# Optimization experiments

Measured on AMD Instinct MI355X. Metric: run time of the kernel, lower is better.

The kernel has to match this reference:

```python
import jax, jax.numpy as jnp
import numpy as np

B, N, K, E, H, V = 128, 256, 4, 300, 150, 32000  # batch, nodes/tree, max children, embed, hidden, vocab
DELTA = 1.0


def setup_inputs() -> dict:
    key = jax.random.key(0)
    ks = jax.random.split(key, 8)
    query = jax.random.randint(ks[0], (B, N), 0, V, dtype=jnp.int32)
    pos = jax.random.randint(ks[1], (B, N), 0, V, dtype=jnp.int32)
    neg = jax.random.randint(ks[2], (B, N), 0, V, dtype=jnp.int32)
    # Complete K-ary tree over N nodes: children of node t are {K*t+1, ..., K*t+K} < N; root = node 0.
    ch = np.full((N, K), -1, dtype=np.int32)
    for t in range(N):
        for j in range(K):
            c = K * t + 1 + j
            if c < N:
                ch[t, j] = c
    children = jnp.asarray(ch)
    emb = jax.random.normal(ks[3], (V, E), dtype=jnp.float32) * 0.02
    W_iou = jax.random.normal(ks[4], (E, 3 * H), dtype=jnp.float32) * 0.05
    U_iou = jax.random.normal(ks[5], (H, 3 * H), dtype=jnp.float32) * 0.05
    b_iou = jnp.zeros((3 * H,), jnp.float32)
    W_f = jax.random.normal(ks[6], (E, H), dtype=jnp.float32) * 0.05
    U_f = jax.random.normal(ks[7], (H, H), dtype=jnp.float32) * 0.05
    b_f = jnp.zeros((H,), jnp.float32)
    return {"query": query, "pos": pos, "neg": neg, "children": children,
            "emb": emb, "W_iou": W_iou, "U_iou": U_iou, "b_iou": b_iou,
            "W_f": W_f, "U_f": U_f, "b_f": b_f}


def _childsum_treelstm(x, children, W_iou, U_iou, b_iou, W_f, U_f, b_f):
    """x: [B, N, E] node embeddings. Returns root (c, h): each [B, H]."""
    Bn, Nn, _ = x.shape
    Hh = U_f.shape[0]
    h0 = jnp.zeros((Bn, Nn, Hh), x.dtype)
    c0 = jnp.zeros((Bn, Nn, Hh), x.dtype)

    def step(carry, t):
        h_all, c_all = carry
        ch = children[t]                        # [K] child indices, -1 = padding
        mask = (ch >= 0)
        idx = jnp.where(mask, ch, 0)
        m = mask.astype(x.dtype)[None, :, None]  # [1, K, 1]
        h_k = h_all[:, idx] * m                 # [B, K, H]
        c_k = c_all[:, idx] * m
        h_sum = h_k.sum(axis=1)                 # child-sum h_tilde [B, H]
        x_t = x[:, t]                           # [B, E]
        iou = x_t @ W_iou + h_sum @ U_iou + b_iou
        i, o, u = jnp.split(iou, 3, axis=-1)
        i = jax.nn.sigmoid(i)
        o = jax.nn.sigmoid(o)
        u = jnp.tanh(u)
        # per-child forget gates: f_jk = sigmoid(W_f x_j + U_f h_k + b_f)
        f = jax.nn.sigmoid((x_t @ W_f + b_f)[:, None, :] + h_k @ U_f)  # [B, K, H]
        c_t = i * u + (f * c_k).sum(axis=1)     # c_k already masked
        h_t = o * jnp.tanh(c_t)
        return (h_all.at[:, t].set(h_t), c_all.at[:, t].set(c_t)), None

    # children have larger indices than parents -> process N-1 .. 0 (root last)
    (h_all, c_all), _ = jax.lax.scan(step, (h0, c0), jnp.arange(Nn - 1, -1, -1))
    return c_all[:, 0], h_all[:, 0]


def _cosine(a, b):
    num = (a * b).sum(-1)
    den = jnp.sqrt((a * a).sum(-1) * (b * b).sum(-1)) + 1e-8
    return num / den


def reference(query, pos, neg, children, emb, W_iou, U_iou, b_iou, W_f, U_f, b_f):
    qc, _ = _childsum_treelstm(emb[query], children, W_iou, U_iou, b_iou, W_f, U_f, b_f)
    pc, _ = _childsum_treelstm(emb[pos], children, W_iou, U_iou, b_iou, W_f, U_f, b_f)
    nc, _ = _childsum_treelstm(emb[neg], children, W_iou, U_iou, b_iou, W_f, U_f, b_f)
    a = _cosine(qc, pc)  # [B]
    b = _cosine(qc, nc)  # [B]
    return jax.nn.relu(DELTA - a + b)
```

## Files before the change

### kernel.cpp

```cpp
#include <hip/hip_runtime.h>
#include <hip/hip_bf16.h>

typedef short short8 __attribute__((ext_vector_type(8)));
typedef float floatx4 __attribute__((ext_vector_type(4)));
typedef unsigned short ushort;

#define Bb 128
#define Nn 256
#define Hh 150
#define HK 160
#define Vv 32000
#define NROW 384
#define PROJC 600
#define NINT 64
#define ZROW (Vv + NROW * NINT)

#define WTN 640

__device__ __forceinline__ float sigf(float x) { return 1.0f / (1.0f + __expf(-x)); }
__device__ __forceinline__ float tanhf_(float x) { return 1.0f - 2.0f / (__expf(2.0f * x) + 1.0f); }
__device__ __forceinline__ float bf2f(ushort s) { union { float f; unsigned u; } v; v.u = ((unsigned)s) << 16; return v.f; }
__device__ __forceinline__ ushort f2bf(float f) { __hip_bfloat16 h = __float2bfloat16(f); return *(ushort*)&h; }

__global__ __launch_bounds__(256) void k_prep(
    const float* __restrict__ W_iou, const float* __restrict__ W_f,
    const float* __restrict__ U_iou, const float* __restrict__ U_f,
    const float* __restrict__ b_iou, const float* __restrict__ b_f,
    short* __restrict__ Wt, short* __restrict__ Uti, short* __restrict__ Utf,
    float* __restrict__ biasw, ushort* __restrict__ h_u, float* __restrict__ c_u)
{
    int idx = blockIdx.x * 256 + threadIdx.x;
    const int nWt = WTN * 320, nUi = 464 * 160, nUf = 160 * 160;
    if (idx < nWt) {
        int n = idx / 320, k = idx % 320;
        float v = 0.f;
        if (k < 300) { if (n < 450) v = W_iou[k * 450 + n]; else if (n < 600) v = W_f[k * 150 + (n - 450)]; }
        Wt[idx] = (short)f2bf(v);
    } else if (idx < nWt + nUi) {
        int i2 = idx - nWt; int n = i2 / 160, k = i2 % 160;
        float v = (k < 150 && n < 450) ? U_iou[k * 450 + n] : 0.f;
        Uti[i2] = (short)f2bf(v);
    } else if (idx < nWt + nUi + nUf) {
        int i2 = idx - nWt - nUi; int n = i2 / 160, k = i2 % 160;
        float v = (k < 150) ? U_f[k * 150 + n] : 0.f;
        Utf[i2] = (short)f2bf(v);
    } else if (idx < nWt + nUi + nUf + WTN) {
        int n = idx - nWt - nUi - nUf;
        biasw[n] = n < 450 ? b_iou[n] : (n < 600 ? b_f[n - 450] : 0.f);
    } else if (idx < nWt + nUi + nUf + WTN + HK) {
        int k = idx - (nWt + nUi + nUf + WTN);
        h_u[(long)ZROW * HK + k] = 0;
        c_u[(long)ZROW * HK + k] = 0.f;
    }
}

__global__ __launch_bounds__(256) void k_vproj(
    const float* __restrict__ emb, const short* __restrict__ Wt,
    const float* __restrict__ biasw, ushort* __restrict__ proj)
{
    __shared__ __align__(16) short As[2][32][328];
    const int tid = threadIdx.x;

    const int bid = blockIdx.x;
    const int xcd = bid & 7, li = bid >> 3;
    const int wgid = (xcd < 4 ? xcd * 63 : 252 + (xcd - 4) * 62) + li;

    const int cg = wgid % 5;
    const int rg = wgid / 5;
    const int rowbase = rg * 320;

    const int w = tid >> 6, lane = tid & 63;
    const int m = lane & 15, kq = (lane >> 4) * 8;
    const int t0 = cg * 8 + w * 2;
    const int col0 = t0 * 16 + m;
    const int col1 = col0 + 16;

    short8 bq0[10], bq1[10];
    #pragma unroll
    for (int ks = 0; ks < 10; ks++) {
        bq0[ks] = *(const short8*)(Wt + (long)col0 * 320 + kq + ks * 32);
        bq1[ks] = *(const short8*)(Wt + (long)col1 * 320 + kq + ks * 32);
    }
    const float bias0 = biasw[col0];
    const float bias1 = biasw[col1];

    for (int i = tid; i < 2 * 32 * 5; i += 256) {
        int bz = i / 160, r2 = (i % 160) / 5, kk = (i % 5) * 4;
        *(short4*)&As[bz][r2][300 + kk] = make_short4(0, 0, 0, 0);
    }

    {
        const float4* src = (const float4*)emb + (long)rowbase * 75;
        for (int i = tid; i < 2400; i += 256) {
            int r = i / 75, k0 = (i % 75) * 4;
            float4 x = src[i];
            short4 sv;
            sv.x = (short)f2bf(x.x); sv.y = (short)f2bf(x.y);
            sv.z = (short)f2bf(x.z); sv.w = (short)f2bf(x.w);
            *(short4*)&As[0][r][k0] = sv;
        }
    }
    __syncthreads();

    for (int c = 0; c < 10; c++) {
        const int buf = c & 1;

        float4 x[10];
        if (c < 9) {
            const float4* src = (const float4*)emb + (long)(rowbase + (c + 1) * 32) * 75;
            #pragma unroll
            for (int j = 0; j < 10; j++) {
                int i = tid + j * 256;
                if (i < 2400) x[j] = src[i];
            }
        }

        floatx4 a00 = {0.f,0.f,0.f,0.f}, a01 = a00, a10 = a00, a11 = a00;
        #pragma unroll
        for (int ks = 0; ks < 10; ks++) {
            short8 a0 = *(const short8*)&As[buf][m][kq + ks * 32];
            short8 a1 = *(const short8*)&As[buf][16 + m][kq + ks * 32];
            a00 = __builtin_amdgcn_mfma_f32_16x16x32_bf16(a0, bq0[ks], a00, 0, 0, 0);
            a01 = __builtin_amdgcn_mfma_f32_16x16x32_bf16(a0, bq1[ks], a01, 0, 0, 0);
            a10 = __builtin_amdgcn_mfma_f32_16x16x32_bf16(a1, bq0[ks], a10, 0, 0, 0);
            a11 = __builtin_amdgcn_mfma_f32_16x16x32_bf16(a1, bq1[ks], a11, 0, 0, 0);
        }

        {
            int v0 = rowbase + c * 32;
            int rb = (lane >> 4) * 4;
            if (col0 < PROJC) {
                #pragma unroll
                for (int reg = 0; reg < 4; reg++) {
                    proj[(long)(v0 + rb + reg) * PROJC + col0]      = f2bf(a00[reg] + bias0);
                    proj[(long)(v0 + 16 + rb + reg) * PROJC + col0] = f2bf(a10[reg] + bias0);
                }
            }
            if (col1 < PROJC) {
                #pragma unroll
                for (int reg = 0; reg < 4; reg++) {
                    proj[(long)(v0 + rb + reg) * PROJC + col1]      = f2bf(a01[reg] + bias1);
                    proj[(long)(v0 + 16 + rb + reg) * PROJC + col1] = f2bf(a11[reg] + bias1);
                }
            }
        }

        if (c < 9) {
            #pragma unroll
            for (int j = 0; j < 10; j++) {
                int i = tid + j * 256;
                if (i < 2400) {
                    int r = i / 75, k0 = (i % 75) * 4;
                    short4 sv;
                    sv.x = (short)f2bf(x[j].x); sv.y = (short)f2bf(x[j].y);
                    sv.z = (short)f2bf(x[j].z); sv.w = (short)f2bf(x[j].w);
                    *(short4*)&As[buf ^ 1][r][k0] = sv;
                }
            }
        }
        __syncthreads();
    }
}

__global__ __launch_bounds__(256) void k_vleaf(
    const ushort* __restrict__ proj, ushort* __restrict__ h_u, float* __restrict__ c_u)
{
    int idx = blockIdx.x * 256 + threadIdx.x;
    int v = idx / 20, k0 = (idx % 20) * 8;
    const ushort* pr = proj + (long)v * PROJC;
    ushort hv[8]; float cvv[8];
    #pragma unroll
    for (int e = 0; e < 8; e++) {
        int k = k0 + e;
        if (k < Hh) {
            float iv = sigf(bf2f(pr[k]));
            float ov = sigf(bf2f(pr[150 + k]));
            float uv = tanhf_(bf2f(pr[300 + k]));
            float cc = iv * uv;
            cvv[e] = cc;
            hv[e] = f2bf(ov * tanhf_(cc));
        } else { cvv[e] = 0.f; hv[e] = 0; }
    }
    *(int4*)(h_u + (long)v * HK + k0) = *(int4*)hv;
    *(float4*)(c_u + (long)v * HK + k0)     = make_float4(cvv[0], cvv[1], cvv[2], cvv[3]);
    *(float4*)(c_u + (long)v * HK + k0 + 4) = make_float4(cvv[4], cvv[5], cvv[6], cvv[7]);
}

__global__ __launch_bounds__(256) void k_level(
    int t_base, int t_cnt,
    const int* __restrict__ tq, const int* __restrict__ tp, const int* __restrict__ tn,
    const int* __restrict__ children, const ushort* __restrict__ proj,
    const short* __restrict__ Uti, const short* __restrict__ Utf,
    ushort* __restrict__ h_u, float* __restrict__ c_u)
{
    __shared__ __align__(16) short As[2][5][16][168];
    __shared__ int idx_s[2][16][4];
    __shared__ int tok_s[2][16];

    const int tid = threadIdx.x;
    const int chunk = blockIdx.x / 24;
    const int r0 = (blockIdx.x % 24) * 16;
    const int tA = t_base + chunk * 2;
    const int nT = min(2, t_base + t_cnt - tA);

    if (tid < 64 * nT) {
        int tt = tid >> 6, q = tid & 63;
        int r = q >> 2, j = q & 3;
        int t = tA + tt;
        int rg = r0 + r, g = rg >> 7, b = rg & 127;
        const int* tok = (g == 0) ? tq : (g == 1 ? tp : tn);
        int ch = children[t * 4 + j];
        int idx;
        if (ch < 0)        idx = ZROW;
        else if (ch >= 64) idx = tok[b * Nn + ch];
        else               idx = Vv + rg * NINT + ch;
        idx_s[tt][r][j] = idx;
        if (j == 0) tok_s[tt][r] = tok[b * Nn + t];
    }
    __syncthreads();

    for (int i = tid; i < 320 * nT; i += 256) {
        int tt = i / 320, i2 = i % 320;
        int r = i2 / 20, k0 = (i2 % 20) * 8;
        int4 v0 = *(const int4*)(h_u + (long)idx_s[tt][r][0] * HK + k0);
        int4 v1 = *(const int4*)(h_u + (long)idx_s[tt][r][1] * HK + k0);
        int4 v2 = *(const int4*)(h_u + (long)idx_s[tt][r][2] * HK + k0);
        int4 v3 = *(const int4*)(h_u + (long)idx_s[tt][r][3] * HK + k0);
        *(int4*)&As[tt][1][r][k0] = v0;
        *(int4*)&As[tt][2][r][k0] = v1;
        *(int4*)&As[tt][3][r][k0] = v2;
        *(int4*)&As[tt][4][r][k0] = v3;
        ushort s[8];
        const ushort* p0 = (const ushort*)&v0; const ushort* p1 = (const ushort*)&v1;
        const ushort* p2 = (const ushort*)&v2; const ushort* p3 = (const ushort*)&v3;
        #pragma unroll
        for (int e = 0; e < 8; e++)
            s[e] = f2bf(bf2f(p0[e]) + bf2f(p1[e]) + bf2f(p2[e]) + bf2f(p3[e]));
        *(int4*)&As[tt][0][r][k0] = *(int4*)s;
    }
    __syncthreads();

    const int w = tid >> 6, lane = tid & 63;
    const int m = lane & 15, kq = (lane >> 4) * 8;
    const int rbase = (lane >> 4) * 4;

    for (int nt = w; nt < 10; nt += 4) {
        int col = nt * 16 + m;

        short8 Bi[5], Bo[5], Bu[5], Bf[5];
        #pragma unroll
        for (int ks = 0; ks < 5; ks++) {
            Bi[ks] = *(const short8*)(Uti + (long)(col)       * HK + kq + ks * 32);
            Bo[ks] = *(const short8*)(Uti + (long)(150 + col) * HK + kq + ks * 32);
            Bu[ks] = *(const short8*)(Uti + (long)(300 + col) * HK + kq + ks * 32);
            Bf[ks] = *(const short8*)(Utf + (long)(col)       * HK + kq + ks * 32);
        }

        for (int tt = 0; tt < nT; ++tt) {
            int t = tA + tt;

            float pv0[4], pv1[4], pv2[4], pv3[4];
            float cu0[4], cu1[4], cu2[4], cu3[4];
            if (col < Hh) {
                #pragma unroll
                for (int reg = 0; reg < 4; reg++) {
                    const ushort* pr = proj + (long)tok_s[tt][rbase + reg] * PROJC;
                    pv0[reg] = bf2f(pr[col]);
                    pv1[reg] = bf2f(pr[150 + col]);
                    pv2[reg] = bf2f(pr[300 + col]);
                    pv3[reg] = bf2f(pr[450 + col]);
                    cu0[reg] = c_u[(long)idx_s[tt][rbase + reg][0] * HK + col];
                    cu1[reg] = c_u[(long)idx_s[tt][rbase + reg][1] * HK + col];
                    cu2[reg] = c_u[(long)idx_s[tt][rbase + reg][2] * HK + col];
                    cu3[reg] = c_u[(long)idx_s[tt][rbase + reg][3] * HK + col];
                }
            }

            floatx4 ai = {0.f,0.f,0.f,0.f}, ao = ai, au = ai;
            floatx4 af0 = ai, af1 = ai, af2 = ai, af3 = ai;
            #pragma unroll
            for (int ks = 0; ks < 5; ks++) {
                short8 asum = *(const short8*)&As[tt][0][m][kq + ks * 32];
                short8 ac0  = *(const short8*)&As[tt][1][m][kq + ks * 32];
                short8 ac1  = *(const short8*)&As[tt][2][m][kq + ks * 32];
                short8 ac2  = *(const short8*)&As[tt][3][m][kq + ks * 32];
                short8 ac3  = *(const short8*)&As[tt][4][m][kq + ks * 32];
                ai  = __builtin_amdgcn_mfma_f32_16x16x32_bf16(asum, Bi[ks], ai, 0, 0, 0);
                ao  = __builtin_amdgcn_mfma_f32_16x16x32_bf16(asum, Bo[ks], ao, 0, 0, 0);
                au  = __builtin_amdgcn_mfma_f32_16x16x32_bf16(asum, Bu[ks], au, 0, 0, 0);
                af0 = __builtin_amdgcn_mfma_f32_16x16x32_bf16(ac0,  Bf[ks], af0, 0, 0, 0);
                af1 = __builtin_amdgcn_mfma_f32_16x16x32_bf16(ac1,  Bf[ks], af1, 0, 0, 0);
                af2 = __builtin_amdgcn_mfma_f32_16x16x32_bf16(ac2,  Bf[ks], af2, 0, 0, 0);
                af3 = __builtin_amdgcn_mfma_f32_16x16x32_bf16(ac3,  Bf[ks], af3, 0, 0, 0);
            }

            if (col < Hh) {
                #pragma unroll
                for (int reg = 0; reg < 4; reg++) {
                    int rg = r0 + rbase + reg;
                    float iv = sigf(pv0[reg] + ai[reg]);
                    float ov = sigf(pv1[reg] + ao[reg]);
                    float uv = tanhf_(pv2[reg] + au[reg]);
                    float fpre = pv3[reg];
                    float cv = iv * uv;
                    cv = fmaf(sigf(fpre + af0[reg]), cu0[reg], cv);
                    cv = fmaf(sigf(fpre + af1[reg]), cu1[reg], cv);
                    cv = fmaf(sigf(fpre + af2[reg]), cu2[reg], cv);
                    cv = fmaf(sigf(fpre + af3[reg]), cu3[reg], cv);
                    long o = (long)(Vv + rg * NINT + t) * HK + col;
                    c_u[o] = cv;
                    h_u[o] = f2bf(ov * tanhf_(cv));
                }
            } else {
                #pragma unroll
                for (int reg = 0; reg < 4; reg++) {
                    long o = (long)(Vv + (r0 + rbase + reg) * NINT + t) * HK + col;
                    c_u[o] = 0.f; h_u[o] = 0;
                }
            }
        }
    }
}

__global__ __launch_bounds__(64) void k_cos(const float* __restrict__ c_u, float* __restrict__ out)
{
    int b = blockIdx.x, tid = threadIdx.x;
    const float* qc = c_u + (long)(Vv + (0 * Bb + b) * NINT) * HK;
    const float* pc = c_u + (long)(Vv + (1 * Bb + b) * NINT) * HK;
    const float* nc = c_u + (long)(Vv + (2 * Bb + b) * NINT) * HK;
    float qp = 0, qn = 0, qq = 0, pp = 0, nn2 = 0;
    for (int k = tid; k < Hh; k += 64) {
        float qv = qc[k], pv = pc[k], nv = nc[k];
        qp += qv * pv; qn += qv * nv; qq += qv * qv; pp += pv * pv; nn2 += nv * nv;
    }
    #pragma unroll
    for (int off = 32; off > 0; off >>= 1) {
        qp += __shfl_down(qp, off, 64);
        qn += __shfl_down(qn, off, 64);
        qq += __shfl_down(qq, off, 64);
        pp += __shfl_down(pp, off, 64);
        nn2 += __shfl_down(nn2, off, 64);
    }
    if (tid == 0) {
        float a = qp / (sqrtf(qq * pp) + 1e-8f);
        float d = qn / (sqrtf(qq * nn2) + 1e-8f);
        out[b] = fmaxf(0.0f, 1.0f - a + d);
    }
}

extern "C" void kernel_launch(void* const* d_in, const int* in_sizes, int n_in,
                              void* d_out, int out_size, void* d_ws, size_t ws_size,
                              hipStream_t stream)
{
    const int*   tq       = (const int*)d_in[0];
    const int*   tp       = (const int*)d_in[1];
    const int*   tn       = (const int*)d_in[2];
    const int*   children = (const int*)d_in[3];
    const float* emb      = (const float*)d_in[4];
    const float* W_iou    = (const float*)d_in[5];
    const float* U_iou    = (const float*)d_in[6];
    const float* b_iou    = (const float*)d_in[7];
    const float* W_f      = (const float*)d_in[8];
    const float* U_f      = (const float*)d_in[9];
    const float* b_f      = (const float*)d_in[10];
    float* out = (float*)d_out;

    char* ws = (char*)d_ws;
    ushort* proj  = (ushort*)ws;
    ushort* h_u   = (ushort*)(ws + 38400000);
    float*  c_u   = (float*)(ws + 56504640);
    short*  Wt    = (short*)(ws + 92713920);
    short*  Uti   = (short*)(ws + 93123520);
    short*  Utf   = (short*)(ws + 93272000);
    float*  biasw = (float*)(ws + 93323200);

    k_prep<<<1194, 256, 0, stream>>>(W_iou, W_f, U_iou, U_f, b_iou, b_f,
                                     Wt, Uti, Utf, biasw, h_u, c_u);
    k_vproj<<<500, 256, 0, stream>>>(emb, Wt, biasw, proj);
    k_vleaf<<<2500, 256, 0, stream>>>(proj, h_u, c_u);
    k_level<<<22 * 24, 256, 0, stream>>>(21, 43, tq, tp, tn, children, proj, Uti, Utf, h_u, c_u);
    k_level<<<8 * 24, 256, 0, stream>>>(5, 16, tq, tp, tn, children, proj, Uti, Utf, h_u, c_u);
    k_level<<<2 * 24, 256, 0, stream>>>(1, 4,  tq, tp, tn, children, proj, Uti, Utf, h_u, c_u);
    k_level<<<1 * 24, 256, 0, stream>>>(0, 1,  tq, tp, tn, children, proj, Uti, Utf, h_u, c_u);
    k_cos<<<Bb, 64, 0, stream>>>(c_u, out);
}
```

Before: 250.2 us.

## Rebalance level-kernel wave work, double vproj grid, coalesce prep reads

The level kernel now splits the flattened (column-tile, node) work units evenly across the four waves. U-weight fragments are reloaded only when a wave's column tile changes, and child/token indices are stored as 16-bit values in shared memory. The vocabulary projection kernel launches twice as many workgroups with half the rows each, using a simpler XCD mapping, to fill more CUs. The weight-prep kernel now reads the source weights along contiguous rows and scatters the transposed writes instead. The intent is to cut wave load imbalance and raise occupancy, at the cost of more redundant B-fragment loads per vproj block and scattered writes in prep.

Result: slower. 255.3 us (+2.1%).

```diff
diff --git a/kernel.cpp b/kernel.cpp
--- a/kernel.cpp
+++ b/kernel.cpp
@@ -30,20 +30,20 @@
     float* __restrict__ biasw, ushort* __restrict__ h_u, float* __restrict__ c_u)
 {
     int idx = blockIdx.x * 256 + threadIdx.x;
-    const int nWt = WTN * 320, nUi = 464 * 160, nUf = 160 * 160;
+    const int nWt = 320 * WTN, nUi = 160 * 464, nUf = 160 * 160;
     if (idx < nWt) {
-        int n = idx / 320, k = idx % 320;
+        int k = idx / WTN, n = idx % WTN;
         float v = 0.f;
         if (k < 300) { if (n < 450) v = W_iou[k * 450 + n]; else if (n < 600) v = W_f[k * 150 + (n - 450)]; }
-        Wt[idx] = (short)f2bf(v);
+        Wt[n * 320 + k] = (short)f2bf(v);
     } else if (idx < nWt + nUi) {
-        int i2 = idx - nWt; int n = i2 / 160, k = i2 % 160;
+        int i2 = idx - nWt; int k = i2 / 464, n = i2 % 464;
         float v = (k < 150 && n < 450) ? U_iou[k * 450 + n] : 0.f;
-        Uti[i2] = (short)f2bf(v);
+        Uti[n * 160 + k] = (short)f2bf(v);
     } else if (idx < nWt + nUi + nUf) {
-        int i2 = idx - nWt - nUi; int n = i2 / 160, k = i2 % 160;
-        float v = (k < 150) ? U_f[k * 150 + n] : 0.f;
-        Utf[i2] = (short)f2bf(v);
+        int i2 = idx - nWt - nUi; int k = i2 / 160, n = i2 % 160;
+        float v = (k < 150 && n < 150) ? U_f[k * 150 + n] : 0.f;
+        Utf[n * 160 + k] = (short)f2bf(v);
     } else if (idx < nWt + nUi + nUf + WTN) {
         int n = idx - nWt - nUi - nUf;
         biasw[n] = n < 450 ? b_iou[n] : (n < 600 ? b_f[n - 450] : 0.f);
@@ -63,11 +63,11 @@
 
     const int bid = blockIdx.x;
     const int xcd = bid & 7, li = bid >> 3;
-    const int wgid = (xcd < 4 ? xcd * 63 : 252 + (xcd - 4) * 62) + li;
+    const int wgid = xcd * 125 + li;
 
     const int cg = wgid % 5;
     const int rg = wgid / 5;
-    const int rowbase = rg * 320;
+    const int rowbase = rg * 160;
 
     const int w = tid >> 6, lane = tid & 63;
     const int m = lane & 15, kq = (lane >> 4) * 8;
@@ -102,11 +102,11 @@
     }
     __syncthreads();
 
-    for (int c = 0; c < 10; c++) {
+    for (int c = 0; c < 5; c++) {
         const int buf = c & 1;
 
         float4 x[10];
-        if (c < 9) {
+        if (c < 4) {
             const float4* src = (const float4*)emb + (long)(rowbase + (c + 1) * 32) * 75;
             #pragma unroll
             for (int j = 0; j < 10; j++) {
@@ -145,7 +145,7 @@
             }
         }
 
-        if (c < 9) {
+        if (c < 4) {
             #pragma unroll
             for (int j = 0; j < 10; j++) {
                 int i = tid + j * 256;
@@ -194,14 +194,34 @@
     ushort* __restrict__ h_u, float* __restrict__ c_u)
 {
     __shared__ __align__(16) short As[2][5][16][168];
-    __shared__ int idx_s[2][16][4];
-    __shared__ int tok_s[2][16];
+    __shared__ ushort idx_s[2][16][4];
+    __shared__ ushort tok_s[2][16];
 
     const int tid = threadIdx.x;
     const int chunk = blockIdx.x / 24;
     const int r0 = (blockIdx.x % 24) * 16;
     const int tA = t_base + chunk * 2;
     const int nT = min(2, t_base + t_cnt - tA);
+
+    const int w = tid >> 6, lane = tid & 63;
+    const int m = lane & 15, kq = (lane >> 4) * 8;
+    const int rbase = (lane >> 4) * 4;
+
+    const int U = 10 * nT;
+    const int u0 = w * U / 4, u1 = (w + 1) * U / 4;
+
+    int cur_nt = u0 / nT;
+    short8 Bi[5], Bo[5], Bu[5], Bf[5];
+    {
+        int colB = cur_nt * 16 + m;
+        #pragma unroll
+        for (int ks = 0; ks < 5; ks++) {
+            Bi[ks] = *(const short8*)(Uti + (long)(colB)       * HK + kq + ks * 32);
+            Bo[ks] = *(const short8*)(Uti + (long)(150 + colB) * HK + kq + ks * 32);
+            Bu[ks] = *(const short8*)(Uti + (long)(300 + colB) * HK + kq + ks * 32);
+            Bf[ks] = *(const short8*)(Utf + (long)(colB)       * HK + kq + ks * 32);
+        }
+    }
 
     if (tid < 64 * nT) {
         int tt = tid >> 6, q = tid & 63;
@@ -214,8 +234,8 @@
         if (ch < 0)        idx = ZROW;
         else if (ch >= 64) idx = tok[b * Nn + ch];
         else               idx = Vv + rg * NINT + ch;
-        idx_s[tt][r][j] = idx;
-        if (j == 0) tok_s[tt][r] = tok[b * Nn + t];
+        idx_s[tt][r][j] = (ushort)idx;
+        if (j == 0) tok_s[tt][r] = (ushort)tok[b * Nn + t];
     }
     __syncthreads();
 
@@ -240,83 +260,80 @@
     }
     __syncthreads();
 
-    const int w = tid >> 6, lane = tid & 63;
-    const int m = lane & 15, kq = (lane >> 4) * 8;
-    const int rbase = (lane >> 4) * 4;
-
-    for (int nt = w; nt < 10; nt += 4) {
+    for (int u = u0; u < u1; ++u) {
+        int nt = u / nT, tt = u - nt * nT;
+        int t = tA + tt;
         int col = nt * 16 + m;
 
-        short8 Bi[5], Bo[5], Bu[5], Bf[5];
+        if (nt != cur_nt) {
+            cur_nt = nt;
+            int colB = nt * 16 + m;
+            #pragma unroll
+            for (int ks = 0; ks < 5; ks++) {
+                Bi[ks] = *(const short8*)(Uti + (long)(colB)       * HK + kq + ks * 32);
+                Bo[ks] = *(const short8*)(Uti + (long)(150 + colB) * HK + kq + ks * 32);
+                Bu[ks] = *(const short8*)(Uti + (long)(300 + colB) * HK + kq + ks * 32);
+                Bf[ks] = *(const short8*)(Utf + (long)(colB)       * HK + kq + ks * 32);
+            }
+        }
+
+        float pv0[4], pv1[4], pv2[4], pv3[4];
+        float cu0[4], cu1[4], cu2[4], cu3[4];
+        if (col < Hh) {
+            #pragma unroll
+            for (int reg = 0; reg < 4; reg++) {
+                const ushort* pr = proj + (long)tok_s[tt][rbase + reg] * PROJC;
+                pv0[reg] = bf2f(pr[col]);
+                pv1[reg] = bf2f(pr[150 + col]);
+                pv2[reg] = bf2f(pr[300 + col]);
+                pv3[reg] = bf2f(pr[450 + col]);
+                cu0[reg] = c_u[(long)idx_s[tt][rbase + reg][0] * HK + col];
+                cu1[reg] = c_u[(long)idx_s[tt][rbase + reg][1] * HK + col];
+                cu2[reg] = c_u[(long)idx_s[tt][rbase + reg][2] * HK + col];
+                cu3[reg] = c_u[(long)idx_s[tt][rbase + reg][3] * HK + col];
+            }
+        }
+
+        floatx4 ai = {0.f,0.f,0.f,0.f}, ao = ai, au = ai;
+        floatx4 af0 = ai, af1 = ai, af2 = ai, af3 = ai;
         #pragma unroll
         for (int ks = 0; ks < 5; ks++) {
-            Bi[ks] = *(const short8*)(Uti + (long)(col)       * HK + kq + ks * 32);
-            Bo[ks] = *(const short8*)(Uti + (long)(150 + col) * HK + kq + ks * 32);
-            Bu[ks] = *(const short8*)(Uti + (long)(300 + col) * HK + kq + ks * 32);
-            Bf[ks] = *(const short8*)(Utf + (long)(col)       * HK + kq + ks * 32);
-        }
-
-        for (int tt = 0; tt < nT; ++tt) {
-            int t = tA + tt;
-
-            float pv0[4], pv1[4], pv2[4], pv3[4];
-            float cu0[4], cu1[4], cu2[4], cu3[4];
-            if (col < Hh) {
-                #pragma unroll
-                for (int reg = 0; reg < 4; reg++) {
-                    const ushort* pr = proj + (long)tok_s[tt][rbase + reg] * PROJC;
-                    pv0[reg] = bf2f(pr[col]);
-                    pv1[reg] = bf2f(pr[150 + col]);
-                    pv2[reg] = bf2f(pr[300 + col]);
-                    pv3[reg] = bf2f(pr[450 + col]);
-                    cu0[reg] = c_u[(long)idx_s[tt][rbase + reg][0] * HK + col];
-                    cu1[reg] = c_u[(long)idx_s[tt][rbase + reg][1] * HK + col];
-                    cu2[reg] = c_u[(long)idx_s[tt][rbase + reg][2] * HK + col];
-                    cu3[reg] = c_u[(long)idx_s[tt][rbase + reg][3] * HK + col];
-                }
-            }
-
-            floatx4 ai = {0.f,0.f,0.f,0.f}, ao = ai, au = ai;
-            floatx4 af0 = ai, af1 = ai, af2 = ai, af3 = ai;
-            #pragma unroll
-            for (int ks = 0; ks < 5; ks++) {
-                short8 asum = *(const short8*)&As[tt][0][m][kq + ks * 32];
-                short8 ac0  = *(const short8*)&As[tt][1][m][kq + ks * 32];
-                short8 ac1  = *(const short8*)&As[tt][2][m][kq + ks * 32];
-                short8 ac2  = *(const short8*)&As[tt][3][m][kq + ks * 32];
-                short8 ac3  = *(const short8*)&As[tt][4][m][kq + ks * 32];
-                ai  = __builtin_amdgcn_mfma_f32_16x16x32_bf16(asum, Bi[ks], ai, 0, 0, 0);
-                ao  = __builtin_amdgcn_mfma_f32_16x16x32_bf16(asum, Bo[ks], ao, 0, 0, 0);
-                au  = __builtin_amdgcn_mfma_f32_16x16x32_bf16(asum, Bu[ks], au, 0, 0, 0);
-                af0 = __builtin_amdgcn_mfma_f32_16x16x32_bf16(ac0,  Bf[ks], af0, 0, 0, 0);
-                af1 = __builtin_amdgcn_mfma_f32_16x16x32_bf16(ac1,  Bf[ks], af1, 0, 0, 0);
-                af2 = __builtin_amdgcn_mfma_f32_16x16x32_bf16(ac2,  Bf[ks], af2, 0, 0, 0);
-                af3 = __builtin_amdgcn_mfma_f32_16x16x32_bf16(ac3,  Bf[ks], af3, 0, 0, 0);
-            }
-
-            if (col < Hh) {
-                #pragma unroll
-                for (int reg = 0; reg < 4; reg++) {
-                    int rg = r0 + rbase + reg;
-                    float iv = sigf(pv0[reg] + ai[reg]);
-                    float ov = sigf(pv1[reg] + ao[reg]);
-                    float uv = tanhf_(pv2[reg] + au[reg]);
-                    float fpre = pv3[reg];
-                    float cv = iv * uv;
-                    cv = fmaf(sigf(fpre + af0[reg]), cu0[reg], cv);
-                    cv = fmaf(sigf(fpre + af1[reg]), cu1[reg], cv);
-                    cv = fmaf(sigf(fpre + af2[reg]), cu2[reg], cv);
-                    cv = fmaf(sigf(fpre + af3[reg]), cu3[reg], cv);
-                    long o = (long)(Vv + rg * NINT + t) * HK + col;
-                    c_u[o] = cv;
-                    h_u[o] = f2bf(ov * tanhf_(cv));
-                }
-            } else {
-                #pragma unroll
-                for (int reg = 0; reg < 4; reg++) {
-                    long o = (long)(Vv + (r0 + rbase + reg) * NINT + t) * HK + col;
-                    c_u[o] = 0.f; h_u[o] = 0;
-                }
+            short8 asum = *(const short8*)&As[tt][0][m][kq + ks * 32];
+            short8 ac0  = *(const short8*)&As[tt][1][m][kq + ks * 32];
+            short8 ac1  = *(const short8*)&As[tt][2][m][kq + ks * 32];
+            short8 ac2  = *(const short8*)&As[tt][3][m][kq + ks * 32];
+            short8 ac3  = *(const short8*)&As[tt][4][m][kq + ks * 32];
+            ai  = __builtin_amdgcn_mfma_f32_16x16x32_bf16(asum, Bi[ks], ai, 0, 0, 0);
+            ao  = __builtin_amdgcn_mfma_f32_16x16x32_bf16(asum, Bo[ks], ao, 0, 0, 0);
+            au  = __builtin_amdgcn_mfma_f32_16x16x32_bf16(asum, Bu[ks], au, 0, 0, 0);
+            af0 = __builtin_amdgcn_mfma_f32_16x16x32_bf16(ac0,  Bf[ks], af0, 0, 0, 0);
+            af1 = __builtin_amdgcn_mfma_f32_16x16x32_bf16(ac1,  Bf[ks], af1, 0, 0, 0);
+            af2 = __builtin_amdgcn_mfma_f32_16x16x32_bf16(ac2,  Bf[ks], af2, 0, 0, 0);
+            af3 = __builtin_amdgcn_mfma_f32_16x16x32_bf16(ac3,  Bf[ks], af3, 0, 0, 0);
+        }
+
+        if (col < Hh) {
+            #pragma unroll
+            for (int reg = 0; reg < 4; reg++) {
+                int rg = r0 + rbase + reg;
+                float iv = sigf(pv0[reg] + ai[reg]);
+                float ov = sigf(pv1[reg] + ao[reg]);
+                float uv = tanhf_(pv2[reg] + au[reg]);
+                float fpre = pv3[reg];
+                float cv = iv * uv;
+                cv = fmaf(sigf(fpre + af0[reg]), cu0[reg], cv);
+                cv = fmaf(sigf(fpre + af1[reg]), cu1[reg], cv);
+                cv = fmaf(sigf(fpre + af2[reg]), cu2[reg], cv);
+                cv = fmaf(sigf(fpre + af3[reg]), cu3[reg], cv);
+                long o = (long)(Vv + rg * NINT + t) * HK + col;
+                c_u[o] = cv;
+                h_u[o] = f2bf(ov * tanhf_(cv));
+            }
+        } else {
+            #pragma unroll
+            for (int reg = 0; reg < 4; reg++) {
+                long o = (long)(Vv + (r0 + rbase + reg) * NINT + t) * HK + col;
+                c_u[o] = 0.f; h_u[o] = 0;
             }
         }
     }
@@ -376,7 +393,7 @@
 
     k_prep<<<1194, 256, 0, stream>>>(W_iou, W_f, U_iou, U_f, b_iou, b_f,
                                      Wt, Uti, Utf, biasw, h_u, c_u);
-    k_vproj<<<500, 256, 0, stream>>>(emb, Wt, biasw, proj);
+    k_vproj<<<1000, 256, 0, stream>>>(emb, Wt, biasw, proj);
     k_vleaf<<<2500, 256, 0, stream>>>(proj, h_u, c_u);
     k_level<<<22 * 24, 256, 0, stream>>>(21, 43, tq, tp, tn, children, proj, Uti, Utf, h_u, c_u);
     k_level<<<8 * 24, 256, 0, stream>>>(5, 16, tq, tp, tn, children, proj, Uti, Utf, h_u, c_u);
```
